# Kernel optimization log

Hardware: AMD Instinct MI355X
Metric: run time of the kernel (lower is better)

Reference implementation:

```python
import jax, jax.numpy as jnp
import numpy as np
import math

B, N, D_IN, D_V, H, D_FF = 8, 2048, 256, 256, 8, 512
HD = D_V // H  # head dim = 32
EPS = 1e-5


def layernorm(x, g, b):
    mu = jnp.mean(x, axis=-1, keepdims=True)
    var = jnp.mean(jnp.square(x - mu), axis=-1, keepdims=True)
    return (x - mu) * jax.lax.rsqrt(var + EPS) * g + b


def setup_inputs() -> dict:
    key = jax.random.key(0)
    ks = jax.random.split(key, 12)
    s = 1.0 / math.sqrt(D_IN)
    return {
        "x": jax.random.normal(ks[0], (B, N, D_IN), jnp.float32),
        "y": jax.random.normal(ks[1], (B, N, D_IN), jnp.float32),
        "Wq": jax.random.normal(ks[2], (D_IN, D_V), jnp.float32) * s,
        "bq": jnp.zeros((D_V,), jnp.float32),
        "Wk": jax.random.normal(ks[3], (D_IN, D_V), jnp.float32) * s,
        "bk": jnp.zeros((D_V,), jnp.float32),
        "Wv": jax.random.normal(ks[4], (D_IN, D_V), jnp.float32) * s,
        "bv": jnp.zeros((D_V,), jnp.float32),
        "W1": jax.random.normal(ks[5], (D_V, D_FF), jnp.float32) * s,
        "b1": jnp.zeros((D_FF,), jnp.float32),
        "W2": jax.random.normal(ks[6], (D_FF, D_V), jnp.float32) * (1.0 / math.sqrt(D_FF)),
        "b2": jnp.zeros((D_V,), jnp.float32),
        "ln0_g": jnp.ones((D_IN,), jnp.float32),
        "ln0_b": jnp.zeros((D_IN,), jnp.float32),
        "ln1_g": jnp.ones((D_V,), jnp.float32),
        "ln1_b": jnp.zeros((D_V,), jnp.float32),
    }


def reference(x, y, Wq, bq, Wk, bk, Wv, bv, W1, b1, W2, b2, ln0_g, ln0_b, ln1_g, ln1_b):
    xn = layernorm(x, ln0_g, ln0_b)                      # ln0 on queries
    Q = (xn @ Wq + bq).reshape(B, N, H, HD)              # [B,Nq,H,hd]
    K = (y @ Wk + bk).reshape(B, N, H, HD)
    V = (y @ Wv + bv).reshape(B, N, H, HD)
    # NOTE: faithful scale = 1/sqrt(dim_V) (full model dim), not head dim
    S = jnp.einsum("bqhd,bkhd->bhqk", Q, K) / math.sqrt(D_V)
    A = jax.nn.softmax(S, axis=-1)
    O = Q + jnp.einsum("bhqk,bkhd->bqhd", A, V)          # per-head residual Q_ + A
    O = O.reshape(B, N, D_V)
    On = layernorm(O, ln1_g, ln1_b)
    ff = jax.nn.gelu(On @ W1 + b1, approximate=False) @ W2 + b2
    return O + ff
```

## Files before the change

### kernel.cpp

```cpp
#include <hip/hip_runtime.h>
#include <math.h>

#define RTOT 16384
#define NSEQ 2048
#define NHEAD 8
#define HDIM 32
#define QSCALE 0.09017132252479462f
#define QINV (1.0f / QSCALE)

typedef __attribute__((ext_vector_type(8))) short short8;
typedef __attribute__((ext_vector_type(4))) float f32x4;
typedef __attribute__((ext_vector_type(4))) unsigned uint4v;

#define GLOBAL_AS(p) ((__attribute__((address_space(1))) void*)(p))
#define LDS_AS(p) ((__attribute__((address_space(3))) void*)(p))

__device__ __forceinline__ unsigned pack_bf16(float a, float b) {
  unsigned ua = __float_as_uint(a) + 0x8000u;
  unsigned ub = __float_as_uint(b) + 0x8000u;
  return (ua >> 16) | (ub & 0xffff0000u);
}
__device__ __forceinline__ unsigned pack_bf16_perm(float a, float b) {
  return __builtin_amdgcn_perm(__float_as_uint(b), __float_as_uint(a),
                               0x07060302u);
}
__device__ __forceinline__ ushort bf16_1(float a) {
  return (ushort)((__float_as_uint(a) + 0x8000u) >> 16);
}
__device__ __forceinline__ float bf16_to_f(ushort u) {
  return __uint_as_float(((unsigned)u) << 16);
}
__device__ __forceinline__ short8 frag4(unsigned a0, unsigned a1, unsigned a2,
                                        unsigned a3) {
  uint4v t = {a0, a1, a2, a3};
  return __builtin_bit_cast(short8, t);
}

__global__ __launch_bounds__(256) void stage0_kernel(
    const float* __restrict__ x, const float* __restrict__ y,
    const float* __restrict__ Wq, const float* __restrict__ Wk,
    const float* __restrict__ Wv, const float* __restrict__ W1,
    const float* __restrict__ W2, const float* __restrict__ ln0g,
    const float* __restrict__ ln0b, ushort* __restrict__ Wqt,
    ushort* __restrict__ Wkt, ushort* __restrict__ Wvt,
    ushort* __restrict__ W1t, ushort* __restrict__ W2t,
    ushort* __restrict__ yh, ushort* __restrict__ xh) {
  const int bid = blockIdx.x;
  const int t = threadIdx.x;
  if (bid < 112) {
    const float* W;
    ushort* Wt;
    int K, N, tile;
    if (bid < 16) { W = Wq; Wt = Wqt; K = 256; N = 256; tile = bid; }
    else if (bid < 32) { W = Wk; Wt = Wkt; K = 256; N = 256; tile = bid - 16; }
    else if (bid < 48) { W = Wv; Wt = Wvt; K = 256; N = 256; tile = bid - 32; }
    else if (bid < 80) { W = W1; Wt = W1t; K = 256; N = 512; tile = bid - 48; }
    else { W = W2; Wt = W2t; K = 512; N = 256; tile = bid - 80; }
    const int tn = N >> 6;
    const int k0 = (tile / tn) << 6, n0 = (tile % tn) << 6;
    __shared__ float T[64][65];
#pragma unroll
    for (int i = 0; i < 16; ++i) {
      const int idx = t + i * 256;
      const int r = idx >> 6, c = idx & 63;
      T[r][c] = W[(size_t)(k0 + r) * N + n0 + c];
    }
    __syncthreads();
#pragma unroll
    for (int i = 0; i < 16; ++i) {
      const int idx = t + i * 256;
      const int r = idx >> 6, c = idx & 63;
      Wt[(size_t)(n0 + r) * K + k0 + c] = bf16_1(T[c][r]);
    }
  } else if (bid < 4208) {
    const size_t i = ((size_t)(bid - 112) * 256 + t) * 4;
    const float4 v = *(const float4*)&y[i];
    uint2 pk;
    pk.x = pack_bf16(v.x, v.y);
    pk.y = pack_bf16(v.z, v.w);
    *(uint2*)&yh[i] = pk;
  } else {
    const int lane = t & 63, wave = t >> 6;
    const size_t row = (size_t)(bid - 4208) * 4 + wave;
    const float* xr = x + row * 256;
    float4 v = *(const float4*)&xr[lane * 4];
    float s = v.x + v.y + v.z + v.w;
#pragma unroll
    for (int m = 1; m < 64; m <<= 1) s += __shfl_xor(s, m, 64);
    const float mu = s * (1.0f / 256.0f);
    const float dx = v.x - mu, dy = v.y - mu, dz = v.z - mu, dw = v.w - mu;
    float ss = dx * dx + dy * dy + dz * dz + dw * dw;
#pragma unroll
    for (int m = 1; m < 64; m <<= 1) ss += __shfl_xor(ss, m, 64);
    const float rstd = rsqrtf(ss * (1.0f / 256.0f) + 1e-5f);
    const float4 gv = *(const float4*)&ln0g[lane * 4];
    const float4 bv = *(const float4*)&ln0b[lane * 4];
    uint2 pk;
    pk.x = pack_bf16(dx * rstd * gv.x + bv.x, dy * rstd * gv.y + bv.y);
    pk.y = pack_bf16(dz * rstd * gv.z + bv.z, dw * rstd * gv.w + bv.w);
    *(uint2*)&xh[row * 256 + lane * 4] = pk;
  }
}

__global__ __launch_bounds__(256) void ln_kernel(
    const float* __restrict__ X, const float* __restrict__ g,
    const float* __restrict__ bt, ushort* __restrict__ Yh) {
  const int lane = threadIdx.x & 63;
  const int wave = threadIdx.x >> 6;
  const size_t row = (size_t)blockIdx.x * 4 + wave;
  const float* xr = X + row * 256;
  float4 v = *(const float4*)&xr[lane * 4];
  float s = v.x + v.y + v.z + v.w;
#pragma unroll
  for (int m = 1; m < 64; m <<= 1) s += __shfl_xor(s, m, 64);
  const float mu = s * (1.0f / 256.0f);
  const float dx = v.x - mu, dy = v.y - mu, dz = v.z - mu, dw = v.w - mu;
  float ss = dx * dx + dy * dy + dz * dz + dw * dw;
#pragma unroll
  for (int m = 1; m < 64; m <<= 1) ss += __shfl_xor(ss, m, 64);
  const float rstd = rsqrtf(ss * (1.0f / 256.0f) + 1e-5f);
  const float4 gv = *(const float4*)&g[lane * 4];
  const float4 bv = *(const float4*)&bt[lane * 4];
  uint2 pk;
  pk.x = pack_bf16(dx * rstd * gv.x + bv.x, dy * rstd * gv.y + bv.y);
  pk.y = pack_bf16(dz * rstd * gv.z + bv.z, dw * rstd * gv.w + bv.w);
  *(uint2*)&Yh[row * 256 + lane * 4] = pk;
}

__global__ __launch_bounds__(256) void qkv_kernel(
    const ushort* __restrict__ xh, const ushort* __restrict__ yh,
    const ushort* __restrict__ Wqt, const ushort* __restrict__ Wkt,
    const ushort* __restrict__ Wvt, const float* __restrict__ bq,
    const float* __restrict__ bk, const float* __restrict__ bv,
    ushort* __restrict__ Qh, ushort* __restrict__ Kh,
    ushort* __restrict__ VhT) {
  __shared__ union UU {
    struct { ushort As[128 * 32]; ushort Bs[64 * 32]; } s;
    ushort Ct[64 * 136];
  } u;
  const int t = threadIdx.x;
  const int lane = t & 63, wave = t >> 6;
  const int l16 = lane & 15, quad = lane >> 4;
  const int row0 = blockIdx.x * 128;
  const int ny = blockIdx.y;
  const int which = ny >> 2;
  const int n0 = (ny & 3) << 6;
  const ushort* A = (which == 2) ? xh : yh;
  const ushort* W = (which == 0) ? Wkt : (which == 1) ? Wvt : Wqt;
  const float* bs = (which == 0) ? bk : (which == 1) ? bv : bq;
  const int mrow = (wave & 1) * 64, ncol = (wave >> 1) * 32;

  const ushort* gA0 = A + (size_t)(row0 + (t >> 2)) * 256 + ((t & 3) << 3);
  const ushort* gA1 = gA0 + (size_t)64 * 256;
  const ushort* gB = W + (size_t)(n0 + (t >> 2)) * 256 + ((t & 3) << 3);
  ushort* lA0 = u.s.As + 8 * t;
  ushort* lA1 = u.s.As + 2048 + 8 * t;
  ushort* lB = u.s.Bs + 8 * t;

  f32x4 acc[4][2] = {};
  for (int kc = 0; kc < 256; kc += 32) {
    __builtin_amdgcn_global_load_lds(GLOBAL_AS(gA0 + kc), LDS_AS(lA0), 16, 0, 0);
    __builtin_amdgcn_global_load_lds(GLOBAL_AS(gA1 + kc), LDS_AS(lA1), 16, 0, 0);
    __builtin_amdgcn_global_load_lds(GLOBAL_AS(gB + kc), LDS_AS(lB), 16, 0, 0);
    __syncthreads();
    short8 af[4], bfr[2];
#pragma unroll
    for (int mi = 0; mi < 4; ++mi)
      af[mi] = *(const short8*)&u.s.As[(mrow + mi * 16 + l16) * 32 + quad * 8];
#pragma unroll
    for (int nj = 0; nj < 2; ++nj)
      bfr[nj] = *(const short8*)&u.s.Bs[(ncol + nj * 16 + l16) * 32 + quad * 8];
#pragma unroll
    for (int mi = 0; mi < 4; ++mi)
#pragma unroll
      for (int nj = 0; nj < 2; ++nj)
        acc[mi][nj] = __builtin_amdgcn_mfma_f32_16x16x32_bf16(
            af[mi], bfr[nj], acc[mi][nj], 0, 0, 0);
    __syncthreads();
  }

  if (which == 1) {
#pragma unroll
    for (int nj = 0; nj < 2; ++nj) {
      const int nloc = ncol + nj * 16 + l16;
      const float bvv = bs[n0 + nloc];
#pragma unroll
      for (int mi = 0; mi < 4; ++mi)
#pragma unroll
        for (int r = 0; r < 4; ++r)
          u.Ct[nloc * 136 + mrow + mi * 16 + quad * 4 + r] =
              bf16_1(acc[mi][nj][r] + bvv);
    }
    __syncthreads();
    const int bb = row0 >> 11, ns0 = row0 & 2047;
#pragma unroll
    for (int i = 0; i < 4; ++i) {
      const int c = t + i * 256;
      const int rr = c >> 4, c8 = (c & 15) << 3;
      *(float4*)&VhT[(size_t)(bb * 256 + n0 + rr) * 2048 + ns0 + c8] =
          *(const float4*)&u.Ct[rr * 136 + c8];
    }
  } else {
#pragma unroll
    for (int nj = 0; nj < 2; ++nj) {
      const int n = n0 + ncol + nj * 16 + l16;
      const float bvv = bs[n];
#pragma unroll
      for (int mi = 0; mi < 4; ++mi) {
#pragma unroll
        for (int r = 0; r < 4; ++r) {
          const size_t m = (size_t)row0 + mrow + mi * 16 + quad * 4 + r;
          const float v = acc[mi][nj][r] + bvv;
          if (which == 2) Qh[m * 256 + n] = bf16_1(v * QSCALE);
          else Kh[m * 256 + n] = bf16_1(v);
        }
      }
    }
  }
}

template <int MODE>
__global__ __launch_bounds__(256) void mgemm_kernel(
    const ushort* __restrict__ A, const ushort* __restrict__ Wt,
    const float* __restrict__ bias, const float* __restrict__ res,
    float* __restrict__ Cf, ushort* __restrict__ Ch, int K, int N) {
  __shared__ ushort As[128 * 32];
  __shared__ ushort Bs[64 * 32];
  const int t = threadIdx.x;
  const int lane = t & 63, wave = t >> 6;
  const int l16 = lane & 15, quad = lane >> 4;
  const int row0 = blockIdx.x * 128;
  const int n0 = blockIdx.y << 6;
  const int mrow = (wave & 1) * 64, ncol = (wave >> 1) * 32;

  const ushort* gA0 = A + (size_t)(row0 + (t >> 2)) * K + ((t & 3) << 3);
  const ushort* gA1 = gA0 + (size_t)64 * K;
  const ushort* gB = Wt + (size_t)(n0 + (t >> 2)) * K + ((t & 3) << 3);
  ushort* lA0 = As + 8 * t;
  ushort* lA1 = As + 2048 + 8 * t;
  ushort* lB = Bs + 8 * t;

  f32x4 acc[4][2] = {};
  for (int kc = 0; kc < K; kc += 32) {
    __builtin_amdgcn_global_load_lds(GLOBAL_AS(gA0 + kc), LDS_AS(lA0), 16, 0, 0);
    __builtin_amdgcn_global_load_lds(GLOBAL_AS(gA1 + kc), LDS_AS(lA1), 16, 0, 0);
    __builtin_amdgcn_global_load_lds(GLOBAL_AS(gB + kc), LDS_AS(lB), 16, 0, 0);
    __syncthreads();
    short8 af[4], bfr[2];
#pragma unroll
    for (int mi = 0; mi < 4; ++mi)
      af[mi] = *(const short8*)&As[(mrow + mi * 16 + l16) * 32 + quad * 8];
#pragma unroll
    for (int nj = 0; nj < 2; ++nj)
      bfr[nj] = *(const short8*)&Bs[(ncol + nj * 16 + l16) * 32 + quad * 8];
#pragma unroll
    for (int mi = 0; mi < 4; ++mi)
#pragma unroll
      for (int nj = 0; nj < 2; ++nj)
        acc[mi][nj] = __builtin_amdgcn_mfma_f32_16x16x32_bf16(
            af[mi], bfr[nj], acc[mi][nj], 0, 0, 0);
    __syncthreads();
  }
#pragma unroll
  for (int nj = 0; nj < 2; ++nj) {
    const int n = n0 + ncol + nj * 16 + l16;
    const float bvv = bias[n];
#pragma unroll
    for (int mi = 0; mi < 4; ++mi) {
#pragma unroll
      for (int r = 0; r < 4; ++r) {
        const size_t m = (size_t)row0 + mrow + mi * 16 + quad * 4 + r;
        float v = acc[mi][nj][r] + bvv;
        if (MODE == 2) {
          v = 0.5f * v * (1.0f + erff(v * 0.70710678118654752f));
          Ch[m * N + n] = bf16_1(v);
        }
        if (MODE == 3) Cf[m * N + n] = v + res[m * N + n];
      }
    }
  }
}

__global__ __launch_bounds__(256) void attn_kernel(
    const ushort* __restrict__ Qh, const ushort* __restrict__ Kh,
    const ushort* __restrict__ VhT, float* __restrict__ O) {
  __shared__ ushort Ks[2][64][40];
  __shared__ ushort Vt[2][32][72];

  const int t = threadIdx.x;
  const int lane = t & 63, wave = t >> 6;
  const int l16 = lane & 15, quad = lane >> 4;
  const int bh = blockIdx.x & 63;
  const int qt = blockIdx.x >> 6;
  const int b = bh >> 3, h = bh & 7;

  const size_t rowQ0 = (size_t)(b * NSEQ + qt * 128 + wave * 32 + l16);
  const short8 qfrag0 = *(const short8*)&Qh[rowQ0 * 256 + h * HDIM + quad * 8];
  const short8 qfrag1 =
      *(const short8*)&Qh[(rowQ0 + 16) * 256 + h * HDIM + quad * 8];
  const short8 ones = {16256, 16256, 16256, 16256,
                       16256, 16256, 16256, 16256};
  const f32x4 zf = {0.f, 0.f, 0.f, 0.f};

  f32x4 o00 = zf, o01 = zf, o10 = zf, o11 = zf;
  f32x4 s0 = zf, s1 = zf;

  const int kr = t >> 2, kc8 = (t & 3) << 3;
  const int krL = (kr & ~12) | ((kr & 4) << 1) | ((kr & 8) >> 1);
  const int vd = t >> 3, vc8 = (t & 7) << 3;
  const ushort* gK = Kh + ((size_t)(b * NSEQ + krL)) * 256 + h * HDIM + kc8;
  const ushort* gV = VhT + ((size_t)(bh * 32 + vd)) * 2048 + vc8;

  float4 kreg = *(const float4*)gK;
  float4 vreg = *(const float4*)gV;

  for (int kt = 0; kt < 32; ++kt) {
    const int bf = kt & 1;
    *(float4*)&Ks[bf][kr][kc8] = kreg;
    *(float4*)&Vt[bf][vd][vc8] = vreg;
    __syncthreads();
    if (kt < 31) {
      kreg = *(const float4*)(gK + (size_t)(kt + 1) * 64 * 256);
      vreg = *(const float4*)(gV + (kt + 1) * 64);
    }

    short8 kf[4];
#pragma unroll
    for (int sub = 0; sub < 4; ++sub)
      kf[sub] = *(const short8*)&Ks[bf][sub * 16 + l16][quad * 8];
    const short8 vf00 = *(const short8*)&Vt[bf][l16][quad * 8];
    const short8 vf01 = *(const short8*)&Vt[bf][l16][32 + quad * 8];
    const short8 vf10 = *(const short8*)&Vt[bf][16 + l16][quad * 8];
    const short8 vf11 = *(const short8*)&Vt[bf][16 + l16][32 + quad * 8];

    f32x4 sa0[4], sa1[4];
#pragma unroll
    for (int sub = 0; sub < 4; ++sub)
      sa0[sub] =
          __builtin_amdgcn_mfma_f32_16x16x32_bf16(kf[sub], qfrag0, zf, 0, 0, 0);
#pragma unroll
    for (int sub = 0; sub < 4; ++sub)
      sa1[sub] =
          __builtin_amdgcn_mfma_f32_16x16x32_bf16(kf[sub], qfrag1, zf, 0, 0, 0);

    unsigned p0[4][2], p1[4][2];
#pragma unroll
    for (int sub = 0; sub < 4; ++sub) {
      p0[sub][0] = pack_bf16_perm(__builtin_amdgcn_exp2f(sa0[sub][0]),
                                  __builtin_amdgcn_exp2f(sa0[sub][1]));
      p0[sub][1] = pack_bf16_perm(__builtin_amdgcn_exp2f(sa0[sub][2]),
                                  __builtin_amdgcn_exp2f(sa0[sub][3]));
    }
#pragma unroll
    for (int sub = 0; sub < 4; ++sub) {
      p1[sub][0] = pack_bf16_perm(__builtin_amdgcn_exp2f(sa1[sub][0]),
                                  __builtin_amdgcn_exp2f(sa1[sub][1]));
      p1[sub][1] = pack_bf16_perm(__builtin_amdgcn_exp2f(sa1[sub][2]),
                                  __builtin_amdgcn_exp2f(sa1[sub][3]));
    }
    unsigned u00 = p0[0][0], w00 = p0[1][0];
    asm("v_permlane32_swap_b32 %0, %1" : "+v"(u00), "+v"(w00));
    unsigned u01 = p0[0][1], w01 = p0[1][1];
    asm("v_permlane32_swap_b32 %0, %1" : "+v"(u01), "+v"(w01));
    unsigned u02 = p0[2][0], w02 = p0[3][0];
    asm("v_permlane32_swap_b32 %0, %1" : "+v"(u02), "+v"(w02));
    unsigned u03 = p0[2][1], w03 = p0[3][1];
    asm("v_permlane32_swap_b32 %0, %1" : "+v"(u03), "+v"(w03));
    const short8 pf00 = frag4(u00, u01, w00, w01);
    const short8 pf01 = frag4(u02, u03, w02, w03);

    unsigned u10 = p1[0][0], w10 = p1[1][0];
    asm("v_permlane32_swap_b32 %0, %1" : "+v"(u10), "+v"(w10));
    unsigned u11 = p1[0][1], w11 = p1[1][1];
    asm("v_permlane32_swap_b32 %0, %1" : "+v"(u11), "+v"(w11));
    unsigned u12 = p1[2][0], w12 = p1[3][0];
    asm("v_permlane32_swap_b32 %0, %1" : "+v"(u12), "+v"(w12));
    unsigned u13 = p1[2][1], w13 = p1[3][1];
    asm("v_permlane32_swap_b32 %0, %1" : "+v"(u13), "+v"(w13));
    const short8 pf10 = frag4(u10, u11, w10, w11);
    const short8 pf11 = frag4(u12, u13, w12, w13);

    o00 = __builtin_amdgcn_mfma_f32_16x16x32_bf16(pf00, vf00, o00, 0, 0, 0);
    o00 = __builtin_amdgcn_mfma_f32_16x16x32_bf16(pf01, vf01, o00, 0, 0, 0);
    o01 = __builtin_amdgcn_mfma_f32_16x16x32_bf16(pf00, vf10, o01, 0, 0, 0);
    o01 = __builtin_amdgcn_mfma_f32_16x16x32_bf16(pf01, vf11, o01, 0, 0, 0);
    o10 = __builtin_amdgcn_mfma_f32_16x16x32_bf16(pf10, vf00, o10, 0, 0, 0);
    o10 = __builtin_amdgcn_mfma_f32_16x16x32_bf16(pf11, vf01, o10, 0, 0, 0);
    o11 = __builtin_amdgcn_mfma_f32_16x16x32_bf16(pf10, vf10, o11, 0, 0, 0);
    o11 = __builtin_amdgcn_mfma_f32_16x16x32_bf16(pf11, vf11, o11, 0, 0, 0);
    s0 = __builtin_amdgcn_mfma_f32_16x16x32_bf16(pf00, ones, s0, 0, 0, 0);
    s0 = __builtin_amdgcn_mfma_f32_16x16x32_bf16(pf01, ones, s0, 0, 0, 0);
    s1 = __builtin_amdgcn_mfma_f32_16x16x32_bf16(pf10, ones, s1, 0, 0, 0);
    s1 = __builtin_amdgcn_mfma_f32_16x16x32_bf16(pf11, ones, s1, 0, 0, 0);
  }

  __syncthreads();
  ushort* sc = (ushort*)Ks + wave * 1280;
  *(short8*)&sc[l16 * 40 + quad * 8] = qfrag0;
  *(short8*)&sc[640 + l16 * 40 + quad * 8] = qfrag1;
  __threadfence_block();
#pragma unroll
  for (int g = 0; g < 2; ++g) {
    const f32x4 oS = g ? s1 : s0;
    const f32x4 oa = g ? o10 : o00;
    const f32x4 ob = g ? o11 : o01;
    const ushort* scg = sc + g * 640;
    const size_t row0 =
        (size_t)(b * NSEQ + qt * 128 + wave * 32 + g * 16 + quad * 4);
#pragma unroll
    for (int r = 0; r < 4; ++r) {
      const float q0 = bf16_to_f(scg[(quad * 4 + r) * 40 + l16]) * QINV;
      const float q1 = bf16_to_f(scg[(quad * 4 + r) * 40 + 16 + l16]) * QINV;
      const float il = 1.0f / oS[r];
      const size_t ro = (row0 + r) * 256 + h * HDIM + l16;
      O[ro] = q0 + oa[r] * il;
      O[ro + 16] = q1 + ob[r] * il;
    }
  }
}

extern "C" void kernel_launch(void* const* d_in, const int* in_sizes, int n_in,
                              void* d_out, int out_size, void* d_ws, size_t ws_size,
                              hipStream_t stream) {
  const float* x = (const float*)d_in[0];
  const float* y = (const float*)d_in[1];
  const float* Wq = (const float*)d_in[2];
  const float* bq = (const float*)d_in[3];
  const float* Wk = (const float*)d_in[4];
  const float* bk = (const float*)d_in[5];
  const float* Wv = (const float*)d_in[6];
  const float* bv = (const float*)d_in[7];
  const float* W1 = (const float*)d_in[8];
  const float* b1 = (const float*)d_in[9];
  const float* W2 = (const float*)d_in[10];
  const float* b2 = (const float*)d_in[11];
  const float* ln0g = (const float*)d_in[12];
  const float* ln0b = (const float*)d_in[13];
  const float* ln1g = (const float*)d_in[14];
  const float* ln1b = (const float*)d_in[15];
  float* out = (float*)d_out;
  char* base = (char*)d_ws;

  const size_t RM = (size_t)RTOT * 256;
  ushort* yh = (ushort*)base;
  float* Ob = (float*)base;
  ushort* Qh = (ushort*)(base + 2 * RM * 4);
  ushort* Kh = (ushort*)(base + 2 * RM * 4 + RM * 2);
  ushort* VhT = (ushort*)(base + 3 * RM * 4);
  ushort* xh = (ushort*)(base + 3 * RM * 4 + RM * 2);
  ushort* Onh = xh;
  ushort* Hidh = Qh;
  char* wbase = base + 4 * RM * 4;
  ushort* Wqt = (ushort*)wbase;
  ushort* Wkt = Wqt + 65536;
  ushort* Wvt = Wkt + 65536;
  ushort* W1t = Wvt + 65536;
  ushort* W2t = W1t + 131072;

  stage0_kernel<<<8304, 256, 0, stream>>>(x, y, Wq, Wk, Wv, W1, W2, ln0g, ln0b,
                                          Wqt, Wkt, Wvt, W1t, W2t, yh, xh);
  qkv_kernel<<<dim3(128, 12), 256, 0, stream>>>(xh, yh, Wqt, Wkt, Wvt, bq, bk,
                                                bv, Qh, Kh, VhT);
  attn_kernel<<<1024, 256, 0, stream>>>(Qh, Kh, VhT, Ob);
  ln_kernel<<<RTOT / 4, 256, 0, stream>>>(Ob, ln1g, ln1b, Onh);
  mgemm_kernel<2><<<dim3(128, 8), 256, 0, stream>>>(Onh, W1t, b1, nullptr,
                                                    nullptr, Hidh, 256, 512);
  mgemm_kernel<3><<<dim3(128, 4), 256, 0, stream>>>(Hidh, W2t, b2, Ob, out,
                                                    nullptr, 512, 256);
}
```

Before: 218.8 us.

## Load K/V attention fragments directly from global memory, one wave per block

```diff
diff --git a/kernel.cpp b/kernel.cpp
--- a/kernel.cpp
+++ b/kernel.cpp
@@ -281,20 +281,16 @@
   }
 }
 
-__global__ __launch_bounds__(256) void attn_kernel(
+__global__ __launch_bounds__(64, 4) void attn_kernel(
     const ushort* __restrict__ Qh, const ushort* __restrict__ Kh,
     const ushort* __restrict__ VhT, float* __restrict__ O) {
-  __shared__ ushort Ks[2][64][40];
-  __shared__ ushort Vt[2][32][72];
-
-  const int t = threadIdx.x;
-  const int lane = t & 63, wave = t >> 6;
+  const int lane = threadIdx.x & 63;
   const int l16 = lane & 15, quad = lane >> 4;
   const int bh = blockIdx.x & 63;
-  const int qt = blockIdx.x >> 6;
+  const int wq = blockIdx.x >> 6;
   const int b = bh >> 3, h = bh & 7;
 
-  const size_t rowQ0 = (size_t)(b * NSEQ + qt * 128 + wave * 32 + l16);
+  const size_t rowQ0 = (size_t)(b * NSEQ + wq * 32 + l16);
   const short8 qfrag0 = *(const short8*)&Qh[rowQ0 * 256 + h * HDIM + quad * 8];
   const short8 qfrag1 =
       *(const short8*)&Qh[(rowQ0 + 16) * 256 + h * HDIM + quad * 8];
@@ -305,58 +301,50 @@
   f32x4 o00 = zf, o01 = zf, o10 = zf, o11 = zf;
   f32x4 s0 = zf, s1 = zf;
 
-  const int kr = t >> 2, kc8 = (t & 3) << 3;
-  const int krL = (kr & ~12) | ((kr & 4) << 1) | ((kr & 8) >> 1);
-  const int vd = t >> 3, vc8 = (t & 7) << 3;
-  const ushort* gK = Kh + ((size_t)(b * NSEQ + krL)) * 256 + h * HDIM + kc8;
-  const ushort* gV = VhT + ((size_t)(bh * 32 + vd)) * 2048 + vc8;
-
-  float4 kreg = *(const float4*)gK;
-  float4 vreg = *(const float4*)gV;
-
-  for (int kt = 0; kt < 32; ++kt) {
-    const int bf = kt & 1;
-    *(float4*)&Ks[bf][kr][kc8] = kreg;
-    *(float4*)&Vt[bf][vd][vc8] = vreg;
-    __syncthreads();
-    if (kt < 31) {
-      kreg = *(const float4*)(gK + (size_t)(kt + 1) * 64 * 256);
-      vreg = *(const float4*)(gV + (kt + 1) * 64);
-    }
-
-    short8 kf[4];
-#pragma unroll
-    for (int sub = 0; sub < 4; ++sub)
-      kf[sub] = *(const short8*)&Ks[bf][sub * 16 + l16][quad * 8];
-    const short8 vf00 = *(const short8*)&Vt[bf][l16][quad * 8];
-    const short8 vf01 = *(const short8*)&Vt[bf][l16][32 + quad * 8];
-    const short8 vf10 = *(const short8*)&Vt[bf][16 + l16][quad * 8];
-    const short8 vf11 = *(const short8*)&Vt[bf][16 + l16][32 + quad * 8];
+  const int swz = (l16 & 3) | ((l16 & 4) << 1) | ((l16 & 8) >> 1);
+  const ushort* gK = Kh + ((size_t)b * NSEQ + swz) * 256 + h * HDIM + quad * 8;
+  const ushort* gV = VhT + ((size_t)(bh * 32 + l16)) * 2048 + quad * 8;
+
+  short8 kfA[4], kfB[4];
+#pragma unroll
+  for (int s = 0; s < 4; ++s)
+    kfA[s] = *(const short8*)(gK + (size_t)(s * 16) * 256);
+
+  auto body = [&](short8* kfc, short8* kfn, int ktc) {
+    const ushort* gv = gV + ktc * 64;
+    const short8 vf00 = *(const short8*)(gv);
+    const short8 vf01 = *(const short8*)(gv + 32);
+    const short8 vf10 = *(const short8*)(gv + 16 * 2048);
+    const short8 vf11 = *(const short8*)(gv + 16 * 2048 + 32);
+    const ushort* gk = gK + (size_t)(ktc + 1) * 64 * 256;
+#pragma unroll
+    for (int s = 0; s < 4; ++s)
+      kfn[s] = *(const short8*)(gk + (size_t)(s * 16) * 256);
 
     f32x4 sa0[4], sa1[4];
 #pragma unroll
-    for (int sub = 0; sub < 4; ++sub)
-      sa0[sub] =
-          __builtin_amdgcn_mfma_f32_16x16x32_bf16(kf[sub], qfrag0, zf, 0, 0, 0);
-#pragma unroll
-    for (int sub = 0; sub < 4; ++sub)
-      sa1[sub] =
-          __builtin_amdgcn_mfma_f32_16x16x32_bf16(kf[sub], qfrag1, zf, 0, 0, 0);
+    for (int s = 0; s < 4; ++s)
+      sa0[s] =
+          __builtin_amdgcn_mfma_f32_16x16x32_bf16(kfc[s], qfrag0, zf, 0, 0, 0);
+#pragma unroll
+    for (int s = 0; s < 4; ++s)
+      sa1[s] =
+          __builtin_amdgcn_mfma_f32_16x16x32_bf16(kfc[s], qfrag1, zf, 0, 0, 0);
 
     unsigned p0[4][2], p1[4][2];
 #pragma unroll
-    for (int sub = 0; sub < 4; ++sub) {
-      p0[sub][0] = pack_bf16_perm(__builtin_amdgcn_exp2f(sa0[sub][0]),
-                                  __builtin_amdgcn_exp2f(sa0[sub][1]));
-      p0[sub][1] = pack_bf16_perm(__builtin_amdgcn_exp2f(sa0[sub][2]),
-                                  __builtin_amdgcn_exp2f(sa0[sub][3]));
-    }
-#pragma unroll
-    for (int sub = 0; sub < 4; ++sub) {
-      p1[sub][0] = pack_bf16_perm(__builtin_amdgcn_exp2f(sa1[sub][0]),
-                                  __builtin_amdgcn_exp2f(sa1[sub][1]));
-      p1[sub][1] = pack_bf16_perm(__builtin_amdgcn_exp2f(sa1[sub][2]),
-                                  __builtin_amdgcn_exp2f(sa1[sub][3]));
+    for (int s = 0; s < 4; ++s) {
+      p0[s][0] = pack_bf16_perm(__builtin_amdgcn_exp2f(sa0[s][0]),
+                                __builtin_amdgcn_exp2f(sa0[s][1]));
+      p0[s][1] = pack_bf16_perm(__builtin_amdgcn_exp2f(sa0[s][2]),
+                                __builtin_amdgcn_exp2f(sa0[s][3]));
+    }
+#pragma unroll
+    for (int s = 0; s < 4; ++s) {
+      p1[s][0] = pack_bf16_perm(__builtin_amdgcn_exp2f(sa1[s][0]),
+                                __builtin_amdgcn_exp2f(sa1[s][1]));
+      p1[s][1] = pack_bf16_perm(__builtin_amdgcn_exp2f(sa1[s][2]),
+                                __builtin_amdgcn_exp2f(sa1[s][3]));
     }
     unsigned u00 = p0[0][0], w00 = p0[1][0];
     asm("v_permlane32_swap_b32 %0, %1" : "+v"(u00), "+v"(w00));
@@ -392,29 +380,25 @@
     s0 = __builtin_amdgcn_mfma_f32_16x16x32_bf16(pf01, ones, s0, 0, 0, 0);
     s1 = __builtin_amdgcn_mfma_f32_16x16x32_bf16(pf10, ones, s1, 0, 0, 0);
     s1 = __builtin_amdgcn_mfma_f32_16x16x32_bf16(pf11, ones, s1, 0, 0, 0);
-  }
-
-  __syncthreads();
-  ushort* sc = (ushort*)Ks + wave * 1280;
-  *(short8*)&sc[l16 * 40 + quad * 8] = qfrag0;
-  *(short8*)&sc[640 + l16 * 40 + quad * 8] = qfrag1;
-  __threadfence_block();
+  };
+
+  for (int kt = 0; kt < 32; kt += 2) {
+    body(kfA, kfB, kt);
+    body(kfB, kfA, kt + 1);
+  }
+
 #pragma unroll
   for (int g = 0; g < 2; ++g) {
     const f32x4 oS = g ? s1 : s0;
     const f32x4 oa = g ? o10 : o00;
     const f32x4 ob = g ? o11 : o01;
-    const ushort* scg = sc + g * 640;
-    const size_t row0 =
-        (size_t)(b * NSEQ + qt * 128 + wave * 32 + g * 16 + quad * 4);
+    const size_t row0 = (size_t)(b * NSEQ + wq * 32 + g * 16 + quad * 4);
 #pragma unroll
     for (int r = 0; r < 4; ++r) {
-      const float q0 = bf16_to_f(scg[(quad * 4 + r) * 40 + l16]) * QINV;
-      const float q1 = bf16_to_f(scg[(quad * 4 + r) * 40 + 16 + l16]) * QINV;
       const float il = 1.0f / oS[r];
       const size_t ro = (row0 + r) * 256 + h * HDIM + l16;
-      O[ro] = q0 + oa[r] * il;
-      O[ro + 16] = q1 + ob[r] * il;
+      O[ro] = bf16_to_f(Qh[ro]) * QINV + oa[r] * il;
+      O[ro + 16] = bf16_to_f(Qh[ro + 16]) * QINV + ob[r] * il;
     }
   }
 }
@@ -461,7 +445,7 @@
                                           Wqt, Wkt, Wvt, W1t, W2t, yh, xh);
   qkv_kernel<<<dim3(128, 12), 256, 0, stream>>>(xh, yh, Wqt, Wkt, Wvt, bq, bk,
                                                 bv, Qh, Kh, VhT);
-  attn_kernel<<<1024, 256, 0, stream>>>(Qh, Kh, VhT, Ob);
+  attn_kernel<<<4096, 64, 0, stream>>>(Qh, Kh, VhT, Ob);
   ln_kernel<<<RTOT / 4, 256, 0, stream>>>(Ob, ln1g, ln1b, Onh);
   mgemm_kernel<2><<<dim3(128, 8), 256, 0, stream>>>(Onh, W1t, b1, nullptr,
                                                     nullptr, Hidh, 256, 512);
```

Result: slower. 280.0 us (+28.0%).

## Split attention keys into two halves with atomic accumulation and fused combine

Applied to the files above, without the earlier changes.

```diff
diff --git a/kernel.cpp b/kernel.cpp
--- a/kernel.cpp
+++ b/kernel.cpp
@@ -44,7 +44,8 @@
     const float* __restrict__ ln0b, ushort* __restrict__ Wqt,
     ushort* __restrict__ Wkt, ushort* __restrict__ Wvt,
     ushort* __restrict__ W1t, ushort* __restrict__ W2t,
-    ushort* __restrict__ yh, ushort* __restrict__ xh) {
+    ushort* __restrict__ yh, ushort* __restrict__ xh,
+    float* __restrict__ zacc) {
   const int bid = blockIdx.x;
   const int t = threadIdx.x;
   if (bid < 112) {
@@ -79,7 +80,7 @@
     pk.x = pack_bf16(v.x, v.y);
     pk.y = pack_bf16(v.z, v.w);
     *(uint2*)&yh[i] = pk;
-  } else {
+  } else if (bid < 8304) {
     const int lane = t & 63, wave = t >> 6;
     const size_t row = (size_t)(bid - 4208) * 4 + wave;
     const float* xr = x + row * 256;
@@ -99,32 +100,47 @@
     pk.x = pack_bf16(dx * rstd * gv.x + bv.x, dy * rstd * gv.y + bv.y);
     pk.y = pack_bf16(dz * rstd * gv.z + bv.z, dw * rstd * gv.w + bv.w);
     *(uint2*)&xh[row * 256 + lane * 4] = pk;
-  }
-}
-
-__global__ __launch_bounds__(256) void ln_kernel(
-    const float* __restrict__ X, const float* __restrict__ g,
+  } else {
+    const float4 z = {0.f, 0.f, 0.f, 0.f};
+    const size_t idx = (size_t)(bid - 8304) * 256 + t;
+    float4* zb = (float4*)zacc;
+#pragma unroll
+    for (int k = 0; k < 4; ++k) zb[idx + (size_t)k * 270336] = z;
+  }
+}
+
+__global__ __launch_bounds__(256) void combine_ln_kernel(
+    const ushort* __restrict__ Qh, float* __restrict__ Oacc,
+    const float* __restrict__ Lacc, const float* __restrict__ g,
     const float* __restrict__ bt, ushort* __restrict__ Yh) {
   const int lane = threadIdx.x & 63;
   const int wave = threadIdx.x >> 6;
   const size_t row = (size_t)blockIdx.x * 4 + wave;
-  const float* xr = X + row * 256;
-  float4 v = *(const float4*)&xr[lane * 4];
-  float s = v.x + v.y + v.z + v.w;
+  const int d0 = lane * 4;
+  float4 o4 = *(const float4*)&Oacc[row * 256 + d0];
+  const float il = 1.0f / Lacc[row * 8 + (lane >> 3)];
+  const uint2 qb = *(const uint2*)&Qh[row * 256 + d0];
+  const float vx = bf16_to_f((ushort)(qb.x & 0xffff)) * QINV + o4.x * il;
+  const float vy = bf16_to_f((ushort)(qb.x >> 16)) * QINV + o4.y * il;
+  const float vz = bf16_to_f((ushort)(qb.y & 0xffff)) * QINV + o4.z * il;
+  const float vw = bf16_to_f((ushort)(qb.y >> 16)) * QINV + o4.w * il;
+  float4 ov = {vx, vy, vz, vw};
+  *(float4*)&Oacc[row * 256 + d0] = ov;
+  float s = vx + vy + vz + vw;
 #pragma unroll
   for (int m = 1; m < 64; m <<= 1) s += __shfl_xor(s, m, 64);
   const float mu = s * (1.0f / 256.0f);
-  const float dx = v.x - mu, dy = v.y - mu, dz = v.z - mu, dw = v.w - mu;
+  const float dx = vx - mu, dy = vy - mu, dz = vz - mu, dw = vw - mu;
   float ss = dx * dx + dy * dy + dz * dz + dw * dw;
 #pragma unroll
   for (int m = 1; m < 64; m <<= 1) ss += __shfl_xor(ss, m, 64);
   const float rstd = rsqrtf(ss * (1.0f / 256.0f) + 1e-5f);
-  const float4 gv = *(const float4*)&g[lane * 4];
-  const float4 bv = *(const float4*)&bt[lane * 4];
+  const float4 gv = *(const float4*)&g[d0];
+  const float4 bv = *(const float4*)&bt[d0];
   uint2 pk;
   pk.x = pack_bf16(dx * rstd * gv.x + bv.x, dy * rstd * gv.y + bv.y);
   pk.y = pack_bf16(dz * rstd * gv.z + bv.z, dw * rstd * gv.w + bv.w);
-  *(uint2*)&Yh[row * 256 + lane * 4] = pk;
+  *(uint2*)&Yh[row * 256 + d0] = pk;
 }
 
 __global__ __launch_bounds__(256) void qkv_kernel(
@@ -283,7 +299,8 @@
 
 __global__ __launch_bounds__(256) void attn_kernel(
     const ushort* __restrict__ Qh, const ushort* __restrict__ Kh,
-    const ushort* __restrict__ VhT, float* __restrict__ O) {
+    const ushort* __restrict__ VhT, float* __restrict__ Oacc,
+    float* __restrict__ Lacc) {
   __shared__ ushort Ks[2][64][40];
   __shared__ ushort Vt[2][32][72];
 
@@ -291,7 +308,9 @@
   const int lane = t & 63, wave = t >> 6;
   const int l16 = lane & 15, quad = lane >> 4;
   const int bh = blockIdx.x & 63;
-  const int qt = blockIdx.x >> 6;
+  const int rest = blockIdx.x >> 6;
+  const int qt = rest & 15;
+  const int half = rest >> 4;
   const int b = bh >> 3, h = bh & 7;
 
   const size_t rowQ0 = (size_t)(b * NSEQ + qt * 128 + wave * 32 + l16);
@@ -308,18 +327,20 @@
   const int kr = t >> 2, kc8 = (t & 3) << 3;
   const int krL = (kr & ~12) | ((kr & 4) << 1) | ((kr & 8) >> 1);
   const int vd = t >> 3, vc8 = (t & 7) << 3;
-  const ushort* gK = Kh + ((size_t)(b * NSEQ + krL)) * 256 + h * HDIM + kc8;
-  const ushort* gV = VhT + ((size_t)(bh * 32 + vd)) * 2048 + vc8;
+  const ushort* gK =
+      Kh + ((size_t)(b * NSEQ + half * 1024 + krL)) * 256 + h * HDIM + kc8;
+  const ushort* gV =
+      VhT + ((size_t)(bh * 32 + vd)) * 2048 + half * 1024 + vc8;
 
   float4 kreg = *(const float4*)gK;
   float4 vreg = *(const float4*)gV;
 
-  for (int kt = 0; kt < 32; ++kt) {
+  for (int kt = 0; kt < 16; ++kt) {
     const int bf = kt & 1;
     *(float4*)&Ks[bf][kr][kc8] = kreg;
     *(float4*)&Vt[bf][vd][vc8] = vreg;
     __syncthreads();
-    if (kt < 31) {
+    if (kt < 15) {
       kreg = *(const float4*)(gK + (size_t)(kt + 1) * 64 * 256);
       vreg = *(const float4*)(gV + (kt + 1) * 64);
     }
@@ -380,6 +401,7 @@
     const short8 pf10 = frag4(u10, u11, w10, w11);
     const short8 pf11 = frag4(u12, u13, w12, w13);
 
+    __builtin_amdgcn_s_setprio(1);
     o00 = __builtin_amdgcn_mfma_f32_16x16x32_bf16(pf00, vf00, o00, 0, 0, 0);
     o00 = __builtin_amdgcn_mfma_f32_16x16x32_bf16(pf01, vf01, o00, 0, 0, 0);
     o01 = __builtin_amdgcn_mfma_f32_16x16x32_bf16(pf00, vf10, o01, 0, 0, 0);
@@ -392,29 +414,22 @@
     s0 = __builtin_amdgcn_mfma_f32_16x16x32_bf16(pf01, ones, s0, 0, 0, 0);
     s1 = __builtin_amdgcn_mfma_f32_16x16x32_bf16(pf10, ones, s1, 0, 0, 0);
     s1 = __builtin_amdgcn_mfma_f32_16x16x32_bf16(pf11, ones, s1, 0, 0, 0);
-  }
-
-  __syncthreads();
-  ushort* sc = (ushort*)Ks + wave * 1280;
-  *(short8*)&sc[l16 * 40 + quad * 8] = qfrag0;
-  *(short8*)&sc[640 + l16 * 40 + quad * 8] = qfrag1;
-  __threadfence_block();
+    __builtin_amdgcn_s_setprio(0);
+  }
+
 #pragma unroll
   for (int g = 0; g < 2; ++g) {
     const f32x4 oS = g ? s1 : s0;
     const f32x4 oa = g ? o10 : o00;
     const f32x4 ob = g ? o11 : o01;
-    const ushort* scg = sc + g * 640;
     const size_t row0 =
         (size_t)(b * NSEQ + qt * 128 + wave * 32 + g * 16 + quad * 4);
 #pragma unroll
     for (int r = 0; r < 4; ++r) {
-      const float q0 = bf16_to_f(scg[(quad * 4 + r) * 40 + l16]) * QINV;
-      const float q1 = bf16_to_f(scg[(quad * 4 + r) * 40 + 16 + l16]) * QINV;
-      const float il = 1.0f / oS[r];
       const size_t ro = (row0 + r) * 256 + h * HDIM + l16;
-      O[ro] = q0 + oa[r] * il;
-      O[ro + 16] = q1 + ob[r] * il;
+      unsafeAtomicAdd(&Oacc[ro], oa[r]);
+      unsafeAtomicAdd(&Oacc[ro + 16], ob[r]);
+      if (l16 == 0) unsafeAtomicAdd(&Lacc[(row0 + r) * 8 + h], oS[r]);
     }
   }
 }
@@ -443,7 +458,8 @@
 
   const size_t RM = (size_t)RTOT * 256;
   ushort* yh = (ushort*)base;
-  float* Ob = (float*)base;
+  float* Lacc = (float*)(base + 16252928);
+  float* Oacc = (float*)(base + 16777216);
   ushort* Qh = (ushort*)(base + 2 * RM * 4);
   ushort* Kh = (ushort*)(base + 2 * RM * 4 + RM * 2);
   ushort* VhT = (ushort*)(base + 3 * RM * 4);
@@ -457,14 +473,16 @@
   ushort* W1t = Wvt + 65536;
   ushort* W2t = W1t + 131072;
 
-  stage0_kernel<<<8304, 256, 0, stream>>>(x, y, Wq, Wk, Wv, W1, W2, ln0g, ln0b,
-                                          Wqt, Wkt, Wvt, W1t, W2t, yh, xh);
+  stage0_kernel<<<9360, 256, 0, stream>>>(x, y, Wq, Wk, Wv, W1, W2, ln0g, ln0b,
+                                          Wqt, Wkt, Wvt, W1t, W2t, yh, xh,
+                                          Lacc);
   qkv_kernel<<<dim3(128, 12), 256, 0, stream>>>(xh, yh, Wqt, Wkt, Wvt, bq, bk,
                                                 bv, Qh, Kh, VhT);
-  attn_kernel<<<1024, 256, 0, stream>>>(Qh, Kh, VhT, Ob);
-  ln_kernel<<<RTOT / 4, 256, 0, stream>>>(Ob, ln1g, ln1b, Onh);
+  attn_kernel<<<2048, 256, 0, stream>>>(Qh, Kh, VhT, Oacc, Lacc);
+  combine_ln_kernel<<<RTOT / 4, 256, 0, stream>>>(Qh, Oacc, Lacc, ln1g, ln1b,
+                                                  Onh);
   mgemm_kernel<2><<<dim3(128, 8), 256, 0, stream>>>(Onh, W1t, b1, nullptr,
                                                     nullptr, Hidh, 256, 512);
-  mgemm_kernel<3><<<dim3(128, 4), 256, 0, stream>>>(Hidh, W2t, b2, Ob, out,
+  mgemm_kernel<3><<<dim3(128, 4), 256, 0, stream>>>(Hidh, W2t, b2, Oacc, out,
                                                     nullptr, 512, 256);
 }
```

New measurement: 244.1 us. +11.6%, slower.

## Double KV tile to 128 keys per barrier, add MFMA priority, reload Q from global

Applied to the files above, without the earlier changes.

```diff
diff --git a/kernel.cpp b/kernel.cpp
--- a/kernel.cpp
+++ b/kernel.cpp
@@ -284,8 +284,8 @@
 __global__ __launch_bounds__(256) void attn_kernel(
     const ushort* __restrict__ Qh, const ushort* __restrict__ Kh,
     const ushort* __restrict__ VhT, float* __restrict__ O) {
-  __shared__ ushort Ks[2][64][40];
-  __shared__ ushort Vt[2][32][72];
+  __shared__ ushort Ks[2][128][40];
+  __shared__ ushort Vt[2][32][136];
 
   const int t = threadIdx.x;
   const int lane = t & 63, wave = t >> 6;
@@ -309,112 +309,120 @@
   const int krL = (kr & ~12) | ((kr & 4) << 1) | ((kr & 8) >> 1);
   const int vd = t >> 3, vc8 = (t & 7) << 3;
   const ushort* gK = Kh + ((size_t)(b * NSEQ + krL)) * 256 + h * HDIM + kc8;
+  const ushort* gK2 = gK + (size_t)64 * 256;
   const ushort* gV = VhT + ((size_t)(bh * 32 + vd)) * 2048 + vc8;
 
-  float4 kreg = *(const float4*)gK;
-  float4 vreg = *(const float4*)gV;
-
-  for (int kt = 0; kt < 32; ++kt) {
+  float4 kreg0 = *(const float4*)gK;
+  float4 kreg1 = *(const float4*)gK2;
+  float4 vreg0 = *(const float4*)gV;
+  float4 vreg1 = *(const float4*)(gV + 64);
+
+  for (int kt = 0; kt < 16; ++kt) {
     const int bf = kt & 1;
-    *(float4*)&Ks[bf][kr][kc8] = kreg;
-    *(float4*)&Vt[bf][vd][vc8] = vreg;
-    __syncthreads();
-    if (kt < 31) {
-      kreg = *(const float4*)(gK + (size_t)(kt + 1) * 64 * 256);
-      vreg = *(const float4*)(gV + (kt + 1) * 64);
-    }
-
-    short8 kf[4];
-#pragma unroll
-    for (int sub = 0; sub < 4; ++sub)
-      kf[sub] = *(const short8*)&Ks[bf][sub * 16 + l16][quad * 8];
-    const short8 vf00 = *(const short8*)&Vt[bf][l16][quad * 8];
-    const short8 vf01 = *(const short8*)&Vt[bf][l16][32 + quad * 8];
-    const short8 vf10 = *(const short8*)&Vt[bf][16 + l16][quad * 8];
-    const short8 vf11 = *(const short8*)&Vt[bf][16 + l16][32 + quad * 8];
-
-    f32x4 sa0[4], sa1[4];
-#pragma unroll
-    for (int sub = 0; sub < 4; ++sub)
-      sa0[sub] =
-          __builtin_amdgcn_mfma_f32_16x16x32_bf16(kf[sub], qfrag0, zf, 0, 0, 0);
-#pragma unroll
-    for (int sub = 0; sub < 4; ++sub)
-      sa1[sub] =
-          __builtin_amdgcn_mfma_f32_16x16x32_bf16(kf[sub], qfrag1, zf, 0, 0, 0);
-
-    unsigned p0[4][2], p1[4][2];
-#pragma unroll
-    for (int sub = 0; sub < 4; ++sub) {
-      p0[sub][0] = pack_bf16_perm(__builtin_amdgcn_exp2f(sa0[sub][0]),
-                                  __builtin_amdgcn_exp2f(sa0[sub][1]));
-      p0[sub][1] = pack_bf16_perm(__builtin_amdgcn_exp2f(sa0[sub][2]),
-                                  __builtin_amdgcn_exp2f(sa0[sub][3]));
-    }
-#pragma unroll
-    for (int sub = 0; sub < 4; ++sub) {
-      p1[sub][0] = pack_bf16_perm(__builtin_amdgcn_exp2f(sa1[sub][0]),
-                                  __builtin_amdgcn_exp2f(sa1[sub][1]));
-      p1[sub][1] = pack_bf16_perm(__builtin_amdgcn_exp2f(sa1[sub][2]),
-                                  __builtin_amdgcn_exp2f(sa1[sub][3]));
-    }
-    unsigned u00 = p0[0][0], w00 = p0[1][0];
-    asm("v_permlane32_swap_b32 %0, %1" : "+v"(u00), "+v"(w00));
-    unsigned u01 = p0[0][1], w01 = p0[1][1];
-    asm("v_permlane32_swap_b32 %0, %1" : "+v"(u01), "+v"(w01));
-    unsigned u02 = p0[2][0], w02 = p0[3][0];
-    asm("v_permlane32_swap_b32 %0, %1" : "+v"(u02), "+v"(w02));
-    unsigned u03 = p0[2][1], w03 = p0[3][1];
-    asm("v_permlane32_swap_b32 %0, %1" : "+v"(u03), "+v"(w03));
-    const short8 pf00 = frag4(u00, u01, w00, w01);
-    const short8 pf01 = frag4(u02, u03, w02, w03);
-
-    unsigned u10 = p1[0][0], w10 = p1[1][0];
-    asm("v_permlane32_swap_b32 %0, %1" : "+v"(u10), "+v"(w10));
-    unsigned u11 = p1[0][1], w11 = p1[1][1];
-    asm("v_permlane32_swap_b32 %0, %1" : "+v"(u11), "+v"(w11));
-    unsigned u12 = p1[2][0], w12 = p1[3][0];
-    asm("v_permlane32_swap_b32 %0, %1" : "+v"(u12), "+v"(w12));
-    unsigned u13 = p1[2][1], w13 = p1[3][1];
-    asm("v_permlane32_swap_b32 %0, %1" : "+v"(u13), "+v"(w13));
-    const short8 pf10 = frag4(u10, u11, w10, w11);
-    const short8 pf11 = frag4(u12, u13, w12, w13);
-
-    o00 = __builtin_amdgcn_mfma_f32_16x16x32_bf16(pf00, vf00, o00, 0, 0, 0);
-    o00 = __builtin_amdgcn_mfma_f32_16x16x32_bf16(pf01, vf01, o00, 0, 0, 0);
-    o01 = __builtin_amdgcn_mfma_f32_16x16x32_bf16(pf00, vf10, o01, 0, 0, 0);
-    o01 = __builtin_amdgcn_mfma_f32_16x16x32_bf16(pf01, vf11, o01, 0, 0, 0);
-    o10 = __builtin_amdgcn_mfma_f32_16x16x32_bf16(pf10, vf00, o10, 0, 0, 0);
-    o10 = __builtin_amdgcn_mfma_f32_16x16x32_bf16(pf11, vf01, o10, 0, 0, 0);
-    o11 = __builtin_amdgcn_mfma_f32_16x16x32_bf16(pf10, vf10, o11, 0, 0, 0);
-    o11 = __builtin_amdgcn_mfma_f32_16x16x32_bf16(pf11, vf11, o11, 0, 0, 0);
-    s0 = __builtin_amdgcn_mfma_f32_16x16x32_bf16(pf00, ones, s0, 0, 0, 0);
-    s0 = __builtin_amdgcn_mfma_f32_16x16x32_bf16(pf01, ones, s0, 0, 0, 0);
-    s1 = __builtin_amdgcn_mfma_f32_16x16x32_bf16(pf10, ones, s1, 0, 0, 0);
-    s1 = __builtin_amdgcn_mfma_f32_16x16x32_bf16(pf11, ones, s1, 0, 0, 0);
-  }
-
-  __syncthreads();
-  ushort* sc = (ushort*)Ks + wave * 1280;
-  *(short8*)&sc[l16 * 40 + quad * 8] = qfrag0;
-  *(short8*)&sc[640 + l16 * 40 + quad * 8] = qfrag1;
-  __threadfence_block();
+    *(float4*)&Ks[bf][kr][kc8] = kreg0;
+    *(float4*)&Ks[bf][64 + kr][kc8] = kreg1;
+    *(float4*)&Vt[bf][vd][vc8] = vreg0;
+    *(float4*)&Vt[bf][vd][64 + vc8] = vreg1;
+    __syncthreads();
+    if (kt < 15) {
+      const size_t ko = (size_t)(kt + 1) * 128 * 256;
+      kreg0 = *(const float4*)(gK + ko);
+      kreg1 = *(const float4*)(gK2 + ko);
+      vreg0 = *(const float4*)(gV + (kt + 1) * 128);
+      vreg1 = *(const float4*)(gV + (kt + 1) * 128 + 64);
+    }
+
+#pragma unroll
+    for (int half = 0; half < 2; ++half) {
+      const int r0 = half * 64;
+      const int c0 = half * 64;
+
+      short8 kf[4];
+#pragma unroll
+      for (int sub = 0; sub < 4; ++sub)
+        kf[sub] = *(const short8*)&Ks[bf][r0 + sub * 16 + l16][quad * 8];
+      const short8 vf00 = *(const short8*)&Vt[bf][l16][c0 + quad * 8];
+      const short8 vf01 = *(const short8*)&Vt[bf][l16][c0 + 32 + quad * 8];
+      const short8 vf10 = *(const short8*)&Vt[bf][16 + l16][c0 + quad * 8];
+      const short8 vf11 = *(const short8*)&Vt[bf][16 + l16][c0 + 32 + quad * 8];
+
+      f32x4 sa0[4], sa1[4];
+#pragma unroll
+      for (int sub = 0; sub < 4; ++sub)
+        sa0[sub] = __builtin_amdgcn_mfma_f32_16x16x32_bf16(kf[sub], qfrag0, zf,
+                                                           0, 0, 0);
+#pragma unroll
+      for (int sub = 0; sub < 4; ++sub)
+        sa1[sub] = __builtin_amdgcn_mfma_f32_16x16x32_bf16(kf[sub], qfrag1, zf,
+                                                           0, 0, 0);
+
+      unsigned p0[4][2], p1[4][2];
+#pragma unroll
+      for (int sub = 0; sub < 4; ++sub) {
+        p0[sub][0] = pack_bf16_perm(__builtin_amdgcn_exp2f(sa0[sub][0]),
+                                    __builtin_amdgcn_exp2f(sa0[sub][1]));
+        p0[sub][1] = pack_bf16_perm(__builtin_amdgcn_exp2f(sa0[sub][2]),
+                                    __builtin_amdgcn_exp2f(sa0[sub][3]));
+      }
+#pragma unroll
+      for (int sub = 0; sub < 4; ++sub) {
+        p1[sub][0] = pack_bf16_perm(__builtin_amdgcn_exp2f(sa1[sub][0]),
+                                    __builtin_amdgcn_exp2f(sa1[sub][1]));
+        p1[sub][1] = pack_bf16_perm(__builtin_amdgcn_exp2f(sa1[sub][2]),
+                                    __builtin_amdgcn_exp2f(sa1[sub][3]));
+      }
+      unsigned u00 = p0[0][0], w00 = p0[1][0];
+      asm("v_permlane32_swap_b32 %0, %1" : "+v"(u00), "+v"(w00));
+      unsigned u01 = p0[0][1], w01 = p0[1][1];
+      asm("v_permlane32_swap_b32 %0, %1" : "+v"(u01), "+v"(w01));
+      unsigned u02 = p0[2][0], w02 = p0[3][0];
+      asm("v_permlane32_swap_b32 %0, %1" : "+v"(u02), "+v"(w02));
+      unsigned u03 = p0[2][1], w03 = p0[3][1];
+      asm("v_permlane32_swap_b32 %0, %1" : "+v"(u03), "+v"(w03));
+      const short8 pf00 = frag4(u00, u01, w00, w01);
+      const short8 pf01 = frag4(u02, u03, w02, w03);
+
+      unsigned u10 = p1[0][0], w10 = p1[1][0];
+      asm("v_permlane32_swap_b32 %0, %1" : "+v"(u10), "+v"(w10));
+      unsigned u11 = p1[0][1], w11 = p1[1][1];
+      asm("v_permlane32_swap_b32 %0, %1" : "+v"(u11), "+v"(w11));
+      unsigned u12 = p1[2][0], w12 = p1[3][0];
+      asm("v_permlane32_swap_b32 %0, %1" : "+v"(u12), "+v"(w12));
+      unsigned u13 = p1[2][1], w13 = p1[3][1];
+      asm("v_permlane32_swap_b32 %0, %1" : "+v"(u13), "+v"(w13));
+      const short8 pf10 = frag4(u10, u11, w10, w11);
+      const short8 pf11 = frag4(u12, u13, w12, w13);
+
+      __builtin_amdgcn_s_setprio(1);
+      o00 = __builtin_amdgcn_mfma_f32_16x16x32_bf16(pf00, vf00, o00, 0, 0, 0);
+      o00 = __builtin_amdgcn_mfma_f32_16x16x32_bf16(pf01, vf01, o00, 0, 0, 0);
+      o01 = __builtin_amdgcn_mfma_f32_16x16x32_bf16(pf00, vf10, o01, 0, 0, 0);
+      o01 = __builtin_amdgcn_mfma_f32_16x16x32_bf16(pf01, vf11, o01, 0, 0, 0);
+      o10 = __builtin_amdgcn_mfma_f32_16x16x32_bf16(pf10, vf00, o10, 0, 0, 0);
+      o10 = __builtin_amdgcn_mfma_f32_16x16x32_bf16(pf11, vf01, o10, 0, 0, 0);
+      o11 = __builtin_amdgcn_mfma_f32_16x16x32_bf16(pf10, vf10, o11, 0, 0, 0);
+      o11 = __builtin_amdgcn_mfma_f32_16x16x32_bf16(pf11, vf11, o11, 0, 0, 0);
+      s0 = __builtin_amdgcn_mfma_f32_16x16x32_bf16(pf00, ones, s0, 0, 0, 0);
+      s0 = __builtin_amdgcn_mfma_f32_16x16x32_bf16(pf01, ones, s0, 0, 0, 0);
+      s1 = __builtin_amdgcn_mfma_f32_16x16x32_bf16(pf10, ones, s1, 0, 0, 0);
+      s1 = __builtin_amdgcn_mfma_f32_16x16x32_bf16(pf11, ones, s1, 0, 0, 0);
+      __builtin_amdgcn_s_setprio(0);
+    }
+  }
+
 #pragma unroll
   for (int g = 0; g < 2; ++g) {
     const f32x4 oS = g ? s1 : s0;
     const f32x4 oa = g ? o10 : o00;
     const f32x4 ob = g ? o11 : o01;
-    const ushort* scg = sc + g * 640;
     const size_t row0 =
         (size_t)(b * NSEQ + qt * 128 + wave * 32 + g * 16 + quad * 4);
 #pragma unroll
     for (int r = 0; r < 4; ++r) {
-      const float q0 = bf16_to_f(scg[(quad * 4 + r) * 40 + l16]) * QINV;
-      const float q1 = bf16_to_f(scg[(quad * 4 + r) * 40 + 16 + l16]) * QINV;
       const float il = 1.0f / oS[r];
       const size_t ro = (row0 + r) * 256 + h * HDIM + l16;
-      O[ro] = q0 + oa[r] * il;
-      O[ro + 16] = q1 + ob[r] * il;
+      O[ro] = bf16_to_f(Qh[ro]) * QINV + oa[r] * il;
+      O[ro + 16] = bf16_to_f(Qh[ro + 16]) * QINV + ob[r] * il;
     }
   }
 }
```

Measured after the change: 216.1 us. About the same (-1.2%).
